# Kernel tuning notes

Hardware: AMD Instinct MI355X
Metric: run time of the kernel (lower is better)

Reference implementation:

```python
import jax, jax.numpy as jnp
import numpy as np

B, T, L = 32, 512, 16   # clips, transitions per clip, IMU samples per transition
C_IN = 6
H1, H2, H3 = 64, 128, 256
OUT = 256
EPS = 1e-5
SLOPE = 0.1


def setup_inputs() -> dict:
    key = jax.random.key(0)
    ks = jax.random.split(key, 24)
    f32 = jnp.float32

    def n(k, shape, s=0.05):
        return jax.random.normal(k, shape, f32) * s

    inp = {
        "imu": jax.random.normal(ks[0], (B, T, L, C_IN), f32),
        # conv block 1
        "w1": n(ks[1], (H1, C_IN, 3)), "b1": n(ks[2], (H1,)),
        "g1": 1.0 + n(ks[3], (H1,)), "be1": n(ks[4], (H1,)),
        "m1": n(ks[5], (H1,)), "v1": jax.random.uniform(ks[6], (H1,), f32, 0.5, 1.5),
        # conv block 2
        "w2": n(ks[7], (H2, H1, 3)), "b2": n(ks[8], (H2,)),
        "g2": 1.0 + n(ks[9], (H2,)), "be2": n(ks[10], (H2,)),
        "m2": n(ks[11], (H2,)), "v2": jax.random.uniform(ks[12], (H2,), f32, 0.5, 1.5),
        # conv block 3
        "w3": n(ks[13], (H3, H2, 3)), "b3": n(ks[14], (H3,)),
        "g3": 1.0 + n(ks[15], (H3,)), "be3": n(ks[16], (H3,)),
        "m3": n(ks[17], (H3,)), "v3": jax.random.uniform(ks[18], (H3,), f32, 0.5, 1.5),
        # projection (torch Linear: y = x @ W.T + b)
        "wp": n(ks[19], (OUT, H3)), "bp": n(ks[20], (OUT,)),
    }
    return inp


def _conv1d(x, w, b):
    # x: [N, C, L], w: [O, I, K], 'same' padding=1 for K=3
    y = jax.lax.conv_general_dilated(
        x, w, window_strides=(1,), padding=[(1, 1)],
        dimension_numbers=("NCH", "OIH", "NCH"))
    return y + b[None, :, None]


def _block(x, w, b, g, be, m, v):
    # Conv1d -> BatchNorm1d (eval, running stats) -> LeakyReLU(0.1); dropout = identity (eval)
    y = _conv1d(x, w, b)
    y = g[None, :, None] * (y - m[None, :, None]) * jax.lax.rsqrt(v + EPS)[None, :, None] + be[None, :, None]
    return jnp.where(y > 0, y, SLOPE * y)


def reference(imu, w1, b1, g1, be1, m1, v1,
              w2, b2, g2, be2, m2, v2,
              w3, b3, g3, be3, m3, v3,
              wp, bp):
    # Flatten the (batch, transition) double loop into one batched pipeline.
    # imu: [B, T, L, 6] -> [B*T, 6, L]  (= .transpose(0,1).unsqueeze(0) per segment)
    x = imu.reshape(B * T, L, C_IN).transpose(0, 2, 1)
    x = _block(x, w1, b1, g1, be1, m1, v1)
    x = _block(x, w2, b2, g2, be2, m2, v2)
    x = _block(x, w3, b3, g3, be3, m3, v3)   # [B*T, 256, L]
    x = jnp.mean(x, axis=-1)                  # AdaptiveAvgPool1d(1) -> [B*T, 256]
    out = x @ wp.T + bp                       # projection -> [B*T, 256]
    return out.reshape(B, T, OUT)
```

## Files before the change

kernel.cpp:

```cpp
#include <hip/hip_runtime.h>
#include <cstdint>
#include <cstddef>


namespace {

typedef __attribute__((ext_vector_type(8))) short short8;
typedef __attribute__((ext_vector_type(4))) float f32x4;

constexpr int NSEG = 32 * 512;
constexpr float kEps = 1e-5f;

constexpr size_t OFF_A2F = 0;
constexpr size_t OFF_A3F = 49152;
constexpr size_t OFF_WP  = 245760;
constexpr size_t OFF_B2  = 376832;
constexpr size_t OFF_B3  = 377344;
constexpr size_t WS_NEED = 378368;

constexpr int L_ACT2 = 20736;
constexpr int L_POOL = 59904;
constexpr int L_TOTAL = 68352;

__device__ __forceinline__ unsigned short f2bf(float f) {
    union { float f; unsigned int u; } a; a.f = f;
    unsigned int u = a.u + 0x7FFFu + ((a.u >> 16) & 1u);
    return (unsigned short)(u >> 16);
}

__device__ __forceinline__ void gll16(const void* g, void* l) {
    __builtin_amdgcn_global_load_lds(
        (const __attribute__((address_space(1))) unsigned int*)g,
        (__attribute__((address_space(3))) unsigned int*)l, 16, 0, 0);
}

__device__ __forceinline__ short8 frag16(const void* p) {
    return __builtin_bit_cast(short8, *(const int4*)p);
}

__global__ __launch_bounds__(256) void k0_prep(
    const float* __restrict__ w2, const float* __restrict__ b2, const float* __restrict__ g2,
    const float* __restrict__ be2, const float* __restrict__ m2, const float* __restrict__ v2,
    const float* __restrict__ w3, const float* __restrict__ b3, const float* __restrict__ g3,
    const float* __restrict__ be3, const float* __restrict__ m3, const float* __restrict__ v3,
    const float* __restrict__ wp, char* __restrict__ ws)
{
    int idx = blockIdx.x * 256 + threadIdx.x;
    if (idx < 3072) {
        int f = idx >> 6, lane = idx & 63;
        int tap = f >> 4, qq = (f >> 3) & 1, rtile = f & 7;
        int row = rtile * 16 + (lane & 15);
        int kb = qq * 32 + (lane >> 4) * 8;
        float a = g2[row] * rsqrtf(v2[row] + kEps);
        unsigned short us[8];
#pragma unroll
        for (int j = 0; j < 8; ++j)
            us[j] = f2bf(a * w2[row * 192 + (kb + j) * 3 + tap]);
        *(int4*)(ws + OFF_A2F + (size_t)idx * 16) = *(const int4*)us;
    } else if (idx < 15360) {
        int u = idx - 3072;
        int f = u >> 6, lane = u & 63;
        int ks = f >> 5, qq = (f >> 4) & 1, rtile = f & 15;
        int tap = ks >> 1, ih = ks & 1;
        int row = rtile * 16 + (lane & 15);
        int kb = qq * 32 + (lane >> 4) * 8;
        float a = g3[row] * rsqrtf(v3[row] + kEps);
        unsigned short us[8];
#pragma unroll
        for (int j = 0; j < 8; ++j) {
            int i = ih * 64 + kb + j;
            us[j] = f2bf(a * w3[row * 384 + i * 3 + tap]);
        }
        *(int4*)(ws + OFF_A3F + (size_t)u * 16) = *(const int4*)us;
    } else if (idx < 23552) {
        int u = idx - 15360;
        int f = u >> 6, lane = u & 63;
        int o = (f >> 3) * 16 + (lane & 15);
        int cb = (f & 7) * 32 + (lane >> 4) * 8;
        unsigned short us[8];
#pragma unroll
        for (int j = 0; j < 8; ++j)
            us[j] = f2bf(wp[o * 256 + cb + j] * 0.0625f);
        *(int4*)(ws + OFF_WP + (size_t)u * 16) = *(const int4*)us;
    } else if (idx < 23680) {
        int o = idx - 23552;
        float a = g2[o] * rsqrtf(v2[o] + kEps);
        ((float*)(ws + OFF_B2))[o] = a * (b2[o] - m2[o]) + be2[o];
    } else if (idx < 23936) {
        int o = idx - 23680;
        float a = g3[o] * rsqrtf(v3[o] + kEps);
        ((float*)(ws + OFF_B3))[o] = a * (b3[o] - m3[o]) + be3[o];
    }
}

__global__ __launch_bounds__(512, 4) void k_all(
    const float* __restrict__ imu,
    const float* __restrict__ w1, const float* __restrict__ b1,
    const float* __restrict__ g1, const float* __restrict__ be1,
    const float* __restrict__ m1, const float* __restrict__ v1,
    const char* __restrict__ ws, const float* __restrict__ bp,
    float* __restrict__ out)
{
    __shared__ char smem[L_TOTAL];
    char* act1L  = smem;
    char* act2L  = smem + L_ACT2;
    char* poolsL = smem + L_POOL;
    char* imuL   = poolsL;
    const char* A2F = ws + OFF_A2F;
    const char* A3F = ws + OFF_A3F;
    const char* WPF = ws + OFF_WP;
    const float* bias2 = (const float*)(ws + OFF_B2);
    const float* bias3 = (const float*)(ws + OFF_B3);

    const int tid = threadIdx.x, lane = tid & 63, wid = tid >> 6;
    const int lo = lane & 15, hi = lane >> 4;
    const int seg0 = blockIdx.x * 8;

    if (wid < 3)
        gll16((const char*)imu + (size_t)seg0 * 384 + wid * 1024 + lane * 16,
              imuL + wid * 1024);
    __syncthreads();

    {
        const float* xf = (const float*)imuL;
        const int c = lane;
        const float a = g1[c] * rsqrtf(v1[c] + kEps);
        const float bb = fmaf(a, b1[c] - m1[c], be1[c]);
        float wk[6][3];
#pragma unroll
        for (int i = 0; i < 6; ++i)
#pragma unroll
            for (int k = 0; k < 3; ++k) wk[i][k] = a * w1[c * 18 + i * 3 + k];

        float acc[16];
#pragma unroll
        for (int l = 0; l < 16; ++l) acc[l] = bb;
#pragma unroll
        for (int i = 0; i < 6; ++i) {
            float x[16];
#pragma unroll
            for (int l = 0; l < 16; ++l) x[l] = xf[wid * 96 + l * 6 + i];
#pragma unroll
            for (int l = 0; l < 16; ++l) {
                float t = wk[i][1] * x[l];
                if (l > 0)  t = fmaf(wk[i][0], x[l - 1], t);
                if (l < 15) t = fmaf(wk[i][2], x[l + 1], t);
                acc[l] += t;
            }
        }
#pragma unroll
        for (int l = 0; l < 16; ++l) {
            float y = acc[l];
            y = y > 0.f ? y : 0.1f * y;
            *(unsigned short*)(act1L + (wid * 18 + l + 1) * 144 + c * 2) = f2bf(y);
        }
        if (tid < 144) {
            int s = tid / 18, rest = tid % 18;
            int h = rest / 9, unit = rest % 9;
            int4 z; z.x = z.y = z.z = z.w = 0;
            *(int4*)(act1L + (s * 18 + h * 17) * 144 + unit * 16) = z;
        }
        if (tid < 272) {
            int s = tid / 34, rest = tid % 34;
            int h = rest / 17, unit = rest % 17;
            int4 z; z.x = z.y = z.z = z.w = 0;
            *(int4*)(act2L + (s * 18 + h * 17) * 272 + unit * 16) = z;
        }
    }
    __syncthreads();

    {
        const int mi = wid >> 1, ni = wid & 1;
        const char* b1base = act1L + lo * 144 + hi * 16;
        f32x4 acc2[2][4];
#pragma unroll
        for (int i = 0; i < 2; ++i)
#pragma unroll
            for (int j = 0; j < 4; ++j) acc2[i][j] = f32x4{0.f, 0.f, 0.f, 0.f};

        short8 a2n[2];
#pragma unroll
        for (int rt = 0; rt < 2; ++rt)
            a2n[rt] = frag16(A2F + (size_t)((mi * 2 + rt) * 64 + lane) * 16);
#pragma unroll
        for (int s = 0; s < 6; ++s) {
            const int tap = s >> 1, qq = s & 1;
            short8 a2c[2]; a2c[0] = a2n[0]; a2c[1] = a2n[1];
            if (s < 5) {
#pragma unroll
                for (int rt = 0; rt < 2; ++rt)
                    a2n[rt] = frag16(A2F + (size_t)(((s + 1) * 8 + mi * 2 + rt) * 64 + lane) * 16);
            }
#pragma unroll
            for (int ct = 0; ct < 4; ++ct) {
                short8 bfr = frag16(b1base + ((ni * 4 + ct) * 18 + tap) * 144 + qq * 64);
                acc2[0][ct] = __builtin_amdgcn_mfma_f32_16x16x32_bf16(a2c[0], bfr, acc2[0][ct], 0, 0, 0);
                acc2[1][ct] = __builtin_amdgcn_mfma_f32_16x16x32_bf16(a2c[1], bfr, acc2[1][ct], 0, 0, 0);
            }
        }
#pragma unroll
        for (int rt = 0; rt < 2; ++rt) {
            int ch0 = (mi * 2 + rt) * 16 + hi * 4;
            float4 b4 = *(const float4*)(bias2 + ch0);
#pragma unroll
            for (int ct = 0; ct < 4; ++ct) {
                float y0 = acc2[rt][ct][0] + b4.x; y0 = y0 > 0.f ? y0 : 0.1f * y0;
                float y1 = acc2[rt][ct][1] + b4.y; y1 = y1 > 0.f ? y1 : 0.1f * y1;
                float y2 = acc2[rt][ct][2] + b4.z; y2 = y2 > 0.f ? y2 : 0.1f * y2;
                float y3 = acc2[rt][ct][3] + b4.w; y3 = y3 > 0.f ? y3 : 0.1f * y3;
                uint2 pk;
                pk.x = (unsigned int)f2bf(y0) | ((unsigned int)f2bf(y1) << 16);
                pk.y = (unsigned int)f2bf(y2) | ((unsigned int)f2bf(y3) << 16);
                *(uint2*)(act2L + ((ni * 4 + ct) * 18 + lo + 1) * 272 + ch0 * 2) = pk;
            }
        }
        if (tid < 264) {
            int row = 8 + tid / 33, unit = tid % 33;
            int4 z; z.x = z.y = z.z = z.w = 0;
            *(int4*)(poolsL + row * 528 + unit * 16) = z;
        }
    }
    __syncthreads();

    {
        const int ni = wid >> 1, mi = wid & 1;
        f32x4 acc3[4][4];
#pragma unroll
        for (int i = 0; i < 4; ++i)
#pragma unroll
            for (int j = 0; j < 4; ++j) acc3[i][j] = f32x4{0.f, 0.f, 0.f, 0.f};

        short8 w3n[4];
#pragma unroll
        for (int ct = 0; ct < 4; ++ct)
            w3n[ct] = frag16(A3F + (size_t)((ni * 4 + ct) * 64 + lane) * 16);
#pragma unroll
        for (int s = 0; s < 12; ++s) {
            const int tap = s >> 2, ih = (s >> 1) & 1, qq = s & 1;
            short8 w3c[4];
#pragma unroll
            for (int ct = 0; ct < 4; ++ct) w3c[ct] = w3n[ct];
            if (s < 11) {
#pragma unroll
                for (int ct = 0; ct < 4; ++ct)
                    w3n[ct] = frag16(A3F + (size_t)(((s + 1) * 16 + ni * 4 + ct) * 64 + lane) * 16);
            }
#pragma unroll
            for (int mt = 0; mt < 4; ++mt) {
                short8 afr = frag16(act2L + ((mi * 4 + mt) * 18 + lo + tap) * 272
                                    + ih * 128 + qq * 64 + hi * 16);
#pragma unroll
                for (int ct = 0; ct < 4; ++ct)
                    acc3[mt][ct] = __builtin_amdgcn_mfma_f32_16x16x32_bf16(
                        afr, w3c[ct], acc3[mt][ct], 0, 0, 0);
            }
        }

#pragma unroll
        for (int ct = 0; ct < 4; ++ct) {
            int co = (ni * 4 + ct) * 16 + lo;
            float bv = bias3[co];
#pragma unroll
            for (int mt = 0; mt < 4; ++mt) {
                float t = 0.f;
#pragma unroll
                for (int r = 0; r < 4; ++r) {
                    float y = acc3[mt][ct][r] + bv;
                    y = y > 0.f ? y : 0.1f * y;
                    t += y;
                }
                t += __shfl_xor(t, 16, 64);
                t += __shfl_xor(t, 32, 64);
                if (hi == 0)
                    *(unsigned short*)(poolsL + (mi * 4 + mt) * 528 + co * 2) = f2bf(t);
            }
        }
    }
    __syncthreads();

    {
        f32x4 acc4[2];
        acc4[0] = f32x4{0.f, 0.f, 0.f, 0.f};
        acc4[1] = f32x4{0.f, 0.f, 0.f, 0.f};
#pragma unroll
        for (int q = 0; q < 8; ++q) {
            short8 pa = frag16(poolsL + lo * 528 + q * 64 + hi * 16);
#pragma unroll
            for (int ct = 0; ct < 2; ++ct) {
                short8 wb = frag16(WPF + (size_t)(((wid * 2 + ct) * 8 + q) * 64 + lane) * 16);
                acc4[ct] = __builtin_amdgcn_mfma_f32_16x16x32_bf16(pa, wb, acc4[ct], 0, 0, 0);
            }
        }
        if (hi < 2) {
#pragma unroll
            for (int ct = 0; ct < 2; ++ct) {
                int o = (wid * 2 + ct) * 16 + lo;
                float bv = bp[o];
#pragma unroll
                for (int r = 0; r < 4; ++r)
                    out[(size_t)(seg0 + hi * 4 + r) * 256 + o] = acc4[ct][r] + bv;
            }
        }
    }
}

}

extern "C" void kernel_launch(void* const* d_in, const int* in_sizes, int n_in,
                              void* d_out, int out_size, void* d_ws, size_t ws_size,
                              hipStream_t stream) {
    if (ws_size < WS_NEED) return;

    const float* imu = (const float*)d_in[0];
    const float* w1 = (const float*)d_in[1];  const float* b1 = (const float*)d_in[2];
    const float* g1 = (const float*)d_in[3];  const float* be1 = (const float*)d_in[4];
    const float* m1 = (const float*)d_in[5];  const float* v1 = (const float*)d_in[6];
    const float* w2 = (const float*)d_in[7];  const float* b2 = (const float*)d_in[8];
    const float* g2 = (const float*)d_in[9];  const float* be2 = (const float*)d_in[10];
    const float* m2 = (const float*)d_in[11]; const float* v2 = (const float*)d_in[12];
    const float* w3 = (const float*)d_in[13]; const float* b3 = (const float*)d_in[14];
    const float* g3 = (const float*)d_in[15]; const float* be3 = (const float*)d_in[16];
    const float* m3 = (const float*)d_in[17]; const float* v3 = (const float*)d_in[18];
    const float* wp = (const float*)d_in[19]; const float* bp = (const float*)d_in[20];
    float* out = (float*)d_out;
    char* ws = (char*)d_ws;

    hipLaunchKernelGGL(k0_prep, dim3(94), dim3(256), 0, stream,
                       w2, b2, g2, be2, m2, v2, w3, b3, g3, be3, m3, v3, wp, ws);
    hipLaunchKernelGGL(k_all, dim3(NSEG / 8), dim3(512), 0, stream,
                       imu, w1, b1, g1, be1, m1, v1, ws, bp, out);
}
```

Before: 90.92 us.

## Double-buffer weight fragments, use lighter barriers, and split pooled values into hi/lo bf16

Replaces __syncthreads with custom waitcnt+barrier helpers and prefetches the global weight fragments for conv2, conv3 and the projection two steps ahead, issuing the loads before the barriers. Conv1 is restructured so each input sample is read once as float2 and scattered into the neighbouring accumulators, and LeakyReLU becomes an fmaxf. The pooled activations are now stored as bf16 high and low parts in the previously zeroed rows 8-15, and the projection MFMA sums both halves with a cross-lane shuffle. This raises projection accuracy, while the extra prefetch registers and the setprio hints aim to hide global-load latency but may raise register pressure.

```diff
diff --git a/kernel.cpp b/kernel.cpp
--- a/kernel.cpp
+++ b/kernel.cpp
@@ -27,6 +27,10 @@
     unsigned int u = a.u + 0x7FFFu + ((a.u >> 16) & 1u);
     return (unsigned short)(u >> 16);
 }
+__device__ __forceinline__ float bf2f(unsigned short h) {
+    union { unsigned int u; float f; } a; a.u = ((unsigned int)h) << 16;
+    return a.f;
+}
 
 __device__ __forceinline__ void gll16(const void* g, void* l) {
     __builtin_amdgcn_global_load_lds(
@@ -37,6 +41,21 @@
 __device__ __forceinline__ short8 frag16(const void* p) {
     return __builtin_bit_cast(short8, *(const int4*)p);
 }
+
+__device__ __forceinline__ void sync_lds() {
+    asm volatile("s_waitcnt lgkmcnt(0)" ::: "memory");
+    __builtin_amdgcn_s_barrier();
+    asm volatile("" ::: "memory");
+    __builtin_amdgcn_sched_barrier(0);
+}
+__device__ __forceinline__ void sync_vm_lds() {
+    asm volatile("s_waitcnt vmcnt(0) lgkmcnt(0)" ::: "memory");
+    __builtin_amdgcn_s_barrier();
+    asm volatile("" ::: "memory");
+    __builtin_amdgcn_sched_barrier(0);
+}
+
+__device__ __forceinline__ float leaky(float y) { return fmaxf(y, 0.1f * y); }
 
 __global__ __launch_bounds__(256) void k0_prep(
     const float* __restrict__ w2, const float* __restrict__ b2, const float* __restrict__ g2,
@@ -119,10 +138,10 @@
     if (wid < 3)
         gll16((const char*)imu + (size_t)seg0 * 384 + wid * 1024 + lane * 16,
               imuL + wid * 1024);
-    __syncthreads();
+    sync_vm_lds();
 
     {
-        const float* xf = (const float*)imuL;
+        const float* xr = (const float*)imuL + wid * 96;
         const int c = lane;
         const float a = g1[c] * rsqrtf(v1[c] + kEps);
         const float bb = fmaf(a, b1[c] - m1[c], be1[c]);
@@ -136,24 +155,22 @@
 #pragma unroll
         for (int l = 0; l < 16; ++l) acc[l] = bb;
 #pragma unroll
-        for (int i = 0; i < 6; ++i) {
-            float x[16];
-#pragma unroll
-            for (int l = 0; l < 16; ++l) x[l] = xf[wid * 96 + l * 6 + i];
-#pragma unroll
-            for (int l = 0; l < 16; ++l) {
-                float t = wk[i][1] * x[l];
-                if (l > 0)  t = fmaf(wk[i][0], x[l - 1], t);
-                if (l < 15) t = fmaf(wk[i][2], x[l + 1], t);
-                acc[l] += t;
-            }
-        }
-#pragma unroll
         for (int l = 0; l < 16; ++l) {
-            float y = acc[l];
-            y = y > 0.f ? y : 0.1f * y;
-            *(unsigned short*)(act1L + (wid * 18 + l + 1) * 144 + c * 2) = f2bf(y);
-        }
+            float2 c01 = *(const float2*)(xr + l * 6);
+            float2 c23 = *(const float2*)(xr + l * 6 + 2);
+            float2 c45 = *(const float2*)(xr + l * 6 + 4);
+            float xs6[6] = {c01.x, c01.y, c23.x, c23.y, c45.x, c45.y};
+#pragma unroll
+            for (int i = 0; i < 6; ++i) {
+                float xv = xs6[i];
+                if (l > 0)  acc[l - 1] = fmaf(wk[i][2], xv, acc[l - 1]);
+                acc[l] = fmaf(wk[i][1], xv, acc[l]);
+                if (l < 15) acc[l + 1] = fmaf(wk[i][0], xv, acc[l + 1]);
+            }
+        }
+#pragma unroll
+        for (int l = 0; l < 16; ++l)
+            *(unsigned short*)(act1L + (wid * 18 + l + 1) * 144 + c * 2) = f2bf(leaky(acc[l]));
         if (tid < 144) {
             int s = tid / 18, rest = tid % 18;
             int h = rest / 9, unit = rest % 9;
@@ -167,116 +184,132 @@
             *(int4*)(act2L + (s * 18 + h * 17) * 272 + unit * 16) = z;
         }
     }
-    __syncthreads();
-
+
+    const int mi2 = wid >> 1, ni2 = wid & 1;
+    short8 a2p[2][2];
+#pragma unroll
+    for (int s = 0; s < 2; ++s)
+#pragma unroll
+        for (int rt = 0; rt < 2; ++rt)
+            a2p[s][rt] = frag16(A2F + (size_t)((s * 8 + mi2 * 2 + rt) * 64 + lane) * 16);
+
+    sync_lds();
+
+    f32x4 acc2[2][4];
+#pragma unroll
+    for (int i = 0; i < 2; ++i)
+#pragma unroll
+        for (int j = 0; j < 4; ++j) acc2[i][j] = f32x4{0.f, 0.f, 0.f, 0.f};
     {
-        const int mi = wid >> 1, ni = wid & 1;
         const char* b1base = act1L + lo * 144 + hi * 16;
-        f32x4 acc2[2][4];
-#pragma unroll
-        for (int i = 0; i < 2; ++i)
-#pragma unroll
-            for (int j = 0; j < 4; ++j) acc2[i][j] = f32x4{0.f, 0.f, 0.f, 0.f};
-
-        short8 a2n[2];
-#pragma unroll
-        for (int rt = 0; rt < 2; ++rt)
-            a2n[rt] = frag16(A2F + (size_t)((mi * 2 + rt) * 64 + lane) * 16);
 #pragma unroll
         for (int s = 0; s < 6; ++s) {
             const int tap = s >> 1, qq = s & 1;
-            short8 a2c[2]; a2c[0] = a2n[0]; a2c[1] = a2n[1];
-            if (s < 5) {
+            short8 bfr[4];
+#pragma unroll
+            for (int ct = 0; ct < 4; ++ct)
+                bfr[ct] = frag16(b1base + ((ni2 * 4 + ct) * 18 + tap) * 144 + qq * 64);
+            __builtin_amdgcn_s_setprio(1);
+#pragma unroll
+            for (int ct = 0; ct < 4; ++ct) {
+                acc2[0][ct] = __builtin_amdgcn_mfma_f32_16x16x32_bf16(a2p[s & 1][0], bfr[ct], acc2[0][ct], 0, 0, 0);
+                acc2[1][ct] = __builtin_amdgcn_mfma_f32_16x16x32_bf16(a2p[s & 1][1], bfr[ct], acc2[1][ct], 0, 0, 0);
+            }
+            __builtin_amdgcn_s_setprio(0);
+            if (s < 4) {
 #pragma unroll
                 for (int rt = 0; rt < 2; ++rt)
-                    a2n[rt] = frag16(A2F + (size_t)(((s + 1) * 8 + mi * 2 + rt) * 64 + lane) * 16);
-            }
-#pragma unroll
-            for (int ct = 0; ct < 4; ++ct) {
-                short8 bfr = frag16(b1base + ((ni * 4 + ct) * 18 + tap) * 144 + qq * 64);
-                acc2[0][ct] = __builtin_amdgcn_mfma_f32_16x16x32_bf16(a2c[0], bfr, acc2[0][ct], 0, 0, 0);
-                acc2[1][ct] = __builtin_amdgcn_mfma_f32_16x16x32_bf16(a2c[1], bfr, acc2[1][ct], 0, 0, 0);
-            }
-        }
-#pragma unroll
-        for (int rt = 0; rt < 2; ++rt) {
-            int ch0 = (mi * 2 + rt) * 16 + hi * 4;
-            float4 b4 = *(const float4*)(bias2 + ch0);
-#pragma unroll
-            for (int ct = 0; ct < 4; ++ct) {
-                float y0 = acc2[rt][ct][0] + b4.x; y0 = y0 > 0.f ? y0 : 0.1f * y0;
-                float y1 = acc2[rt][ct][1] + b4.y; y1 = y1 > 0.f ? y1 : 0.1f * y1;
-                float y2 = acc2[rt][ct][2] + b4.z; y2 = y2 > 0.f ? y2 : 0.1f * y2;
-                float y3 = acc2[rt][ct][3] + b4.w; y3 = y3 > 0.f ? y3 : 0.1f * y3;
-                uint2 pk;
-                pk.x = (unsigned int)f2bf(y0) | ((unsigned int)f2bf(y1) << 16);
-                pk.y = (unsigned int)f2bf(y2) | ((unsigned int)f2bf(y3) << 16);
-                *(uint2*)(act2L + ((ni * 4 + ct) * 18 + lo + 1) * 272 + ch0 * 2) = pk;
-            }
-        }
-        if (tid < 264) {
-            int row = 8 + tid / 33, unit = tid % 33;
-            int4 z; z.x = z.y = z.z = z.w = 0;
-            *(int4*)(poolsL + row * 528 + unit * 16) = z;
-        }
-    }
-    __syncthreads();
-
+                    a2p[s & 1][rt] = frag16(A2F + (size_t)(((s + 2) * 8 + mi2 * 2 + rt) * 64 + lane) * 16);
+            }
+        }
+    }
+
+    const int ni3 = wid >> 1, mi3 = wid & 1;
+    short8 w3p[2][4];
+#pragma unroll
+    for (int s = 0; s < 2; ++s)
+#pragma unroll
+        for (int ct = 0; ct < 4; ++ct)
+            w3p[s][ct] = frag16(A3F + (size_t)((s * 16 + ni3 * 4 + ct) * 64 + lane) * 16);
+
+#pragma unroll
+    for (int rt = 0; rt < 2; ++rt) {
+        int ch0 = (mi2 * 2 + rt) * 16 + hi * 4;
+        float4 b4 = *(const float4*)(bias2 + ch0);
+#pragma unroll
+        for (int ct = 0; ct < 4; ++ct) {
+            float y0 = leaky(acc2[rt][ct][0] + b4.x);
+            float y1 = leaky(acc2[rt][ct][1] + b4.y);
+            float y2 = leaky(acc2[rt][ct][2] + b4.z);
+            float y3 = leaky(acc2[rt][ct][3] + b4.w);
+            uint2 pk;
+            pk.x = (unsigned int)f2bf(y0) | ((unsigned int)f2bf(y1) << 16);
+            pk.y = (unsigned int)f2bf(y2) | ((unsigned int)f2bf(y3) << 16);
+            *(uint2*)(act2L + ((ni2 * 4 + ct) * 18 + lo + 1) * 272 + ch0 * 2) = pk;
+        }
+    }
+    sync_lds();
+
+    f32x4 acc3[4][4];
+#pragma unroll
+    for (int i = 0; i < 4; ++i)
+#pragma unroll
+        for (int j = 0; j < 4; ++j) acc3[i][j] = f32x4{0.f, 0.f, 0.f, 0.f};
     {
-        const int ni = wid >> 1, mi = wid & 1;
-        f32x4 acc3[4][4];
-#pragma unroll
-        for (int i = 0; i < 4; ++i)
-#pragma unroll
-            for (int j = 0; j < 4; ++j) acc3[i][j] = f32x4{0.f, 0.f, 0.f, 0.f};
-
-        short8 w3n[4];
-#pragma unroll
-        for (int ct = 0; ct < 4; ++ct)
-            w3n[ct] = frag16(A3F + (size_t)((ni * 4 + ct) * 64 + lane) * 16);
 #pragma unroll
         for (int s = 0; s < 12; ++s) {
             const int tap = s >> 2, ih = (s >> 1) & 1, qq = s & 1;
-            short8 w3c[4];
-#pragma unroll
-            for (int ct = 0; ct < 4; ++ct) w3c[ct] = w3n[ct];
-            if (s < 11) {
-#pragma unroll
-                for (int ct = 0; ct < 4; ++ct)
-                    w3n[ct] = frag16(A3F + (size_t)(((s + 1) * 16 + ni * 4 + ct) * 64 + lane) * 16);
-            }
-#pragma unroll
-            for (int mt = 0; mt < 4; ++mt) {
-                short8 afr = frag16(act2L + ((mi * 4 + mt) * 18 + lo + tap) * 272
-                                    + ih * 128 + qq * 64 + hi * 16);
+            short8 afr[4];
+#pragma unroll
+            for (int mt = 0; mt < 4; ++mt)
+                afr[mt] = frag16(act2L + ((mi3 * 4 + mt) * 18 + lo + tap) * 272
+                                 + ih * 128 + qq * 64 + hi * 16);
+            __builtin_amdgcn_s_setprio(1);
+#pragma unroll
+            for (int mt = 0; mt < 4; ++mt)
 #pragma unroll
                 for (int ct = 0; ct < 4; ++ct)
                     acc3[mt][ct] = __builtin_amdgcn_mfma_f32_16x16x32_bf16(
-                        afr, w3c[ct], acc3[mt][ct], 0, 0, 0);
-            }
-        }
-
-#pragma unroll
-        for (int ct = 0; ct < 4; ++ct) {
-            int co = (ni * 4 + ct) * 16 + lo;
-            float bv = bias3[co];
-#pragma unroll
-            for (int mt = 0; mt < 4; ++mt) {
-                float t = 0.f;
-#pragma unroll
-                for (int r = 0; r < 4; ++r) {
-                    float y = acc3[mt][ct][r] + bv;
-                    y = y > 0.f ? y : 0.1f * y;
-                    t += y;
-                }
-                t += __shfl_xor(t, 16, 64);
-                t += __shfl_xor(t, 32, 64);
-                if (hi == 0)
-                    *(unsigned short*)(poolsL + (mi * 4 + mt) * 528 + co * 2) = f2bf(t);
-            }
-        }
-    }
-    __syncthreads();
+                        afr[mt], w3p[s & 1][ct], acc3[mt][ct], 0, 0, 0);
+            __builtin_amdgcn_s_setprio(0);
+            if (s < 10) {
+#pragma unroll
+                for (int ct = 0; ct < 4; ++ct)
+                    w3p[s & 1][ct] = frag16(A3F + (size_t)(((s + 2) * 16 + ni3 * 4 + ct) * 64 + lane) * 16);
+            }
+        }
+    }
+
+#pragma unroll
+    for (int ct = 0; ct < 4; ++ct) {
+        int co = (ni3 * 4 + ct) * 16 + lo;
+        float bv = bias3[co];
+#pragma unroll
+        for (int mt = 0; mt < 4; ++mt) {
+            float t = 0.f;
+#pragma unroll
+            for (int r = 0; r < 4; ++r)
+                t += leaky(acc3[mt][ct][r] + bv);
+            t += __shfl_xor(t, 16, 64);
+            t += __shfl_xor(t, 32, 64);
+            if (hi == 0) {
+                unsigned short ph = f2bf(t);
+                unsigned short pl = f2bf(t - bf2f(ph));
+                int row = mi3 * 4 + mt;
+                *(unsigned short*)(poolsL + row * 528 + co * 2) = ph;
+                *(unsigned short*)(poolsL + (row + 8) * 528 + co * 2) = pl;
+            }
+        }
+    }
+
+    short8 wbp[2][2];
+#pragma unroll
+    for (int q = 0; q < 2; ++q)
+#pragma unroll
+        for (int ct = 0; ct < 2; ++ct)
+            wbp[q][ct] = frag16(WPF + (size_t)(((wid * 2 + ct) * 8 + q) * 64 + lane) * 16);
+
+    sync_lds();
 
     {
         f32x4 acc4[2];
@@ -285,20 +318,23 @@
 #pragma unroll
         for (int q = 0; q < 8; ++q) {
             short8 pa = frag16(poolsL + lo * 528 + q * 64 + hi * 16);
-#pragma unroll
-            for (int ct = 0; ct < 2; ++ct) {
-                short8 wb = frag16(WPF + (size_t)(((wid * 2 + ct) * 8 + q) * 64 + lane) * 16);
-                acc4[ct] = __builtin_amdgcn_mfma_f32_16x16x32_bf16(pa, wb, acc4[ct], 0, 0, 0);
-            }
-        }
-        if (hi < 2) {
-#pragma unroll
-            for (int ct = 0; ct < 2; ++ct) {
-                int o = (wid * 2 + ct) * 16 + lo;
-                float bv = bp[o];
-#pragma unroll
-                for (int r = 0; r < 4; ++r)
-                    out[(size_t)(seg0 + hi * 4 + r) * 256 + o] = acc4[ct][r] + bv;
+            acc4[0] = __builtin_amdgcn_mfma_f32_16x16x32_bf16(pa, wbp[q & 1][0], acc4[0], 0, 0, 0);
+            acc4[1] = __builtin_amdgcn_mfma_f32_16x16x32_bf16(pa, wbp[q & 1][1], acc4[1], 0, 0, 0);
+            if (q < 6) {
+#pragma unroll
+                for (int ct = 0; ct < 2; ++ct)
+                    wbp[q & 1][ct] = frag16(WPF + (size_t)(((wid * 2 + ct) * 8 + q + 2) * 64 + lane) * 16);
+            }
+        }
+#pragma unroll
+        for (int ct = 0; ct < 2; ++ct) {
+            int o = (wid * 2 + ct) * 16 + lo;
+            float bv = bp[o];
+#pragma unroll
+            for (int r = 0; r < 4; ++r) {
+                float t = acc4[ct][r] + __shfl_xor(acc4[ct][r], 32, 64);
+                if (hi < 2)
+                    out[(size_t)(seg0 + hi * 4 + r) * 256 + o] = t + bv;
             }
         }
     }
```

After: 85.86 us. -5.6%, faster.
